# Performance work log

Hardware: AMD Instinct MI355X
Metric: run time of the kernel (lower is better)

Reference implementation:

```python
import jax, jax.numpy as jnp
import numpy as np

VOCAB, EMB, HID = 50000, 256, 512
BATCH, SEQ = 128, 512


def setup_inputs() -> dict:
    key = jax.random.key(0)
    k1, k2, k3, k4 = jax.random.split(key, 4)
    tokens = jax.random.randint(k1, (BATCH, SEQ), 0, VOCAB, dtype=jnp.int32)
    V = jax.random.normal(k2, (VOCAB, EMB), dtype=jnp.float32) * 0.05
    W = jax.random.normal(k3, (EMB + HID, HID), dtype=jnp.float32) * (1.0 / np.sqrt(EMB + HID))
    b = jnp.zeros((HID,), dtype=jnp.float32)
    Wd = jax.random.normal(k4, (HID, 1), dtype=jnp.float32) * (1.0 / np.sqrt(HID))
    bd = jnp.zeros((1,), dtype=jnp.float32)
    return {"tokens": tokens, "V": V, "W": W, "b": b, "Wd": Wd, "bd": bd}


def reference(tokens, V, W, b, Wd, bd):
    # embedding lookup: [B, S, E]
    x = V[tokens]
    B = x.shape[0]
    # tanh RNN over time: state_t = tanh([x_t, state_{t-1}] @ W + b)
    Wx, Wh = W[:EMB], W[EMB:]  # concat-matmul == split matmuls
    xs = jnp.einsum('bse,eh->bsh', x, Wx)  # precompute input projections

    def step(state, x_proj):
        state = jnp.tanh(x_proj + state @ Wh + b)
        return state, None

    init = jnp.zeros((B, HID), dtype=x.dtype)
    final_state, _ = jax.lax.scan(step, init, jnp.swapaxes(xs, 0, 1))
    # dense head -> [B]
    y = final_state @ Wd + bd
    return y.reshape(-1)
```

## Files before the change

kernel.cpp:

```cpp
#include <hip/hip_runtime.h>

#define EMBD 256
#define HIDD 512
#define SEQL 512
#define NCOL 512
#define CGC  64
#define THR  512
#define NRING 64
#define RPW  2

typedef unsigned int u32;
typedef unsigned long long u64;
typedef _Float16 h2 __attribute__((ext_vector_type(2)));

#define WS_W16_OFF 0
#define WS_X_OFF   (768 * 1024)

static __device__ __forceinline__ float dot2(u32 a, u32 b, float c) {
#if __has_builtin(__builtin_amdgcn_fdot2)
    return __builtin_amdgcn_fdot2(__builtin_bit_cast(h2, a), __builtin_bit_cast(h2, b), c, false);
#else
    h2 ha = __builtin_bit_cast(h2, a), hb = __builtin_bit_cast(h2, b);
    float r = fmaf((float)ha.x, (float)hb.x, c);
    return fmaf((float)ha.y, (float)hb.y, r);
#endif
}

static __device__ __forceinline__ u32 packh2(float a, float b) {
    _Float16 lo = (_Float16)a, hi = (_Float16)b;
    return (u32)__builtin_bit_cast(unsigned short, lo)
         | ((u32)__builtin_bit_cast(unsigned short, hi) << 16);
}

__global__ __launch_bounds__(1024)
void init_X(u64* __restrict__ X) {
    X[(size_t)blockIdx.x * 1024 + threadIdx.x] = 0ull;
}

__global__ __launch_bounds__(256)
void convert_W(const float* __restrict__ W, u32* __restrict__ W16) {
    int idx = blockIdx.x * 256 + threadIdx.x;
    if (idx >= 384 * NCOL) return;
    int kp = idx >> 9, c = idx & 511;
    float lo = W[(size_t)(2 * kp) * NCOL + c];
    float hi = W[(size_t)(2 * kp + 1) * NCOL + c];
    W16[idx] = packh2(lo, hi);
}

__global__ __launch_bounds__(THR, 1)
void rnn_ring(const int*   __restrict__ tokens,
              const float* __restrict__ V,
              const u32*   __restrict__ W16,
              const float* __restrict__ bias,
              const float* __restrict__ Wd,
              const float* __restrict__ bd,
              float*       __restrict__ y,
              u64*         __restrict__ X)
{
    __shared__ __align__(16) u32 vcA[RPW][384];
    __shared__ __align__(16) u32 vcB[RPW][384];
    __shared__ float partA[RPW][CGC][9];
    __shared__ float partB[RPW][CGC][9];
    __shared__ int   toks[4][SEQL];
    __shared__ float yred[8];

    const int tid  = threadIdx.x;
    const int wg   = blockIdx.x;
    const int pr   = wg >> 3;
    const int cg   = wg & 7;
    const int ringA = 2 * pr;
    const int wv   = tid >> 6;
    const int lane = tid & 63;
    const int gc   = cg * CGC + lane;
    const int row0 = pr * 4;

    for (int i = tid; i < 4 * SEQL; i += THR)
        toks[i >> 9][i & 511] = tokens[(row0 + (i >> 9)) * SEQL + (i & 511)];
    for (int i = tid; i < RPW * 256; i += THR) {
        vcA[i >> 8][128 + (i & 255)] = 0u;
        vcB[i >> 8][128 + (i & 255)] = 0u;
    }

    u32 we[16], ws[32];
    #pragma unroll
    for (int i = 0; i < 16; ++i) we[i] = W16[(size_t)(wv * 16 + i) * NCOL + gc];
    #pragma unroll
    for (int j = 0; j < 32; ++j) ws[j] = W16[(size_t)(128 + wv * 32 + j) * NCOL + gc];

    __syncthreads();

    const int er = tid >> 7, ee = tid & 127;
    {
        int tok = toks[er][0];
        float2 ev = *(const float2*)&V[(size_t)tok * EMBD + 2 * ee];
        u32 dw = packh2(ev.x, ev.y);
        if (er < 2) vcA[er][ee] = dw; else vcB[er - 2][ee] = dw;
    }
    __syncthreads();

    const float bias_r = (tid < 256) ? bias[cg * CGC + (tid & 63)] : 0.f;
    const int  lrow = lane >> 5, lpair = lane & 31;
    const bool own  = (wv == cg);
    const int  ringsel = tid >> 7, rrow = (tid >> 6) & 1, rcol = tid & 63;

    for (int t = 0; t < SEQL; ++t) {
        u64* XA = X + (((size_t)((t + 1) & 1) * NRING + ringA    ) * RPW + lrow) * 256 + wv * 32 + lpair;
        u64* XB = X + (((size_t)((t + 1) & 1) * NRING + ringA + 1) * RPW + lrow) * 256 + wv * 32 + lpair;
        u64 vA = 0, vB = 0;
        if (!own) {
            vA = __hip_atomic_load(XA, __ATOMIC_RELAXED, __HIP_MEMORY_SCOPE_AGENT);
            vB = __hip_atomic_load(XB, __ATOMIC_RELAXED, __HIP_MEMORY_SCOPE_AGENT);
        }

        const int tn   = (t + 1 < SEQL) ? (t + 1) : (SEQL - 1);
        const int tokn = toks[er][tn];
        const float2 ev = *(const float2*)&V[(size_t)tokn * EMBD + 2 * ee];

        float a0 = 0.f, a1 = 0.f, b0 = 0.f, b1 = 0.f;
        {
            const uint4* pa0 = (const uint4*)&vcA[0][wv * 16];
            const uint4* pa1 = (const uint4*)&vcA[1][wv * 16];
            const uint4* pb0 = (const uint4*)&vcB[0][wv * 16];
            const uint4* pb1 = (const uint4*)&vcB[1][wv * 16];
            #pragma unroll
            for (int j = 0; j < 4; ++j) {
                uint4 xa0 = pa0[j], xa1 = pa1[j], xb0 = pb0[j], xb1 = pb1[j];
                a0 = dot2(xa0.x, we[4*j+0], a0); a0 = dot2(xa0.y, we[4*j+1], a0);
                a0 = dot2(xa0.z, we[4*j+2], a0); a0 = dot2(xa0.w, we[4*j+3], a0);
                a1 = dot2(xa1.x, we[4*j+0], a1); a1 = dot2(xa1.y, we[4*j+1], a1);
                a1 = dot2(xa1.z, we[4*j+2], a1); a1 = dot2(xa1.w, we[4*j+3], a1);
                b0 = dot2(xb0.x, we[4*j+0], b0); b0 = dot2(xb0.y, we[4*j+1], b0);
                b0 = dot2(xb0.z, we[4*j+2], b0); b0 = dot2(xb0.w, we[4*j+3], b0);
                b1 = dot2(xb1.x, we[4*j+0], b1); b1 = dot2(xb1.y, we[4*j+1], b1);
                b1 = dot2(xb1.z, we[4*j+2], b1); b1 = dot2(xb1.w, we[4*j+3], b1);
            }
        }

        if (!own) {
            if (!__all((u32)(vA >> 32) == (u32)t)) {
                do {
                    __builtin_amdgcn_s_sleep(1);
                    vA = __hip_atomic_load(XA, __ATOMIC_RELAXED, __HIP_MEMORY_SCOPE_AGENT);
                } while (!__all((u32)(vA >> 32) == (u32)t));
            }
            vcA[lrow][128 + wv * 32 + lpair] = (u32)vA;
        }
        {
            const uint4* p0 = (const uint4*)&vcA[0][128 + wv * 32];
            const uint4* p1 = (const uint4*)&vcA[1][128 + wv * 32];
            #pragma unroll
            for (int j = 0; j < 8; ++j) {
                uint4 x0 = p0[j], x1 = p1[j];
                a0 = dot2(x0.x, ws[4*j+0], a0); a0 = dot2(x0.y, ws[4*j+1], a0);
                a0 = dot2(x0.z, ws[4*j+2], a0); a0 = dot2(x0.w, ws[4*j+3], a0);
                a1 = dot2(x1.x, ws[4*j+0], a1); a1 = dot2(x1.y, ws[4*j+1], a1);
                a1 = dot2(x1.z, ws[4*j+2], a1); a1 = dot2(x1.w, ws[4*j+3], a1);
            }
        }
        partA[0][lane][wv] = a0;
        partA[1][lane][wv] = a1;

        if (!own) {
            if (!__all((u32)(vB >> 32) == (u32)t)) {
                do {
                    __builtin_amdgcn_s_sleep(1);
                    vB = __hip_atomic_load(XB, __ATOMIC_RELAXED, __HIP_MEMORY_SCOPE_AGENT);
                } while (!__all((u32)(vB >> 32) == (u32)t));
            }
            vcB[lrow][128 + wv * 32 + lpair] = (u32)vB;
        }
        {
            const uint4* p0 = (const uint4*)&vcB[0][128 + wv * 32];
            const uint4* p1 = (const uint4*)&vcB[1][128 + wv * 32];
            #pragma unroll
            for (int j = 0; j < 8; ++j) {
                uint4 x0 = p0[j], x1 = p1[j];
                b0 = dot2(x0.x, ws[4*j+0], b0); b0 = dot2(x0.y, ws[4*j+1], b0);
                b0 = dot2(x0.z, ws[4*j+2], b0); b0 = dot2(x0.w, ws[4*j+3], b0);
                b1 = dot2(x1.x, ws[4*j+0], b1); b1 = dot2(x1.y, ws[4*j+1], b1);
                b1 = dot2(x1.z, ws[4*j+2], b1); b1 = dot2(x1.w, ws[4*j+3], b1);
            }
        }
        partB[0][lane][wv] = b0;
        partB[1][lane][wv] = b1;

        __syncthreads();

        if (tid < 256) {
            const float* P = ringsel ? &partB[rrow][rcol][0] : &partA[rrow][rcol][0];
            float s = P[0] + P[1] + P[2] + P[3] + P[4] + P[5] + P[6] + P[7] + bias_r;
            s = tanhf(s);
            float snb = __shfl_down(s, 1);
            if ((rcol & 1) == 0) {
                const int gp = cg * 32 + (rcol >> 1);
                u32 dw = packh2(s, snb);
                if (ringsel == 0) vcA[rrow][128 + gp] = dw;
                else              vcB[rrow][128 + gp] = dw;
                u64 pk = (u64)dw | ((u64)(u32)(t + 1) << 32);
                u64* dst = X + (((size_t)(t & 1) * NRING + ringA + ringsel) * RPW + rrow) * 256 + gp;
                __hip_atomic_store(dst, pk, __ATOMIC_RELAXED, __HIP_MEMORY_SCOPE_AGENT);
            }
        }
        {
            u32 dw = packh2(ev.x, ev.y);
            if (er < 2) vcA[er][ee] = dw; else vcB[er - 2][ee] = dw;
        }
        __syncthreads();
    }

    if (cg == 0) {
        if (wv != 0) {
            u64* XA = X + (((size_t)((SEQL - 1) & 1) * NRING + ringA    ) * RPW + lrow) * 256 + wv * 32 + lpair;
            u64* XB = X + (((size_t)((SEQL - 1) & 1) * NRING + ringA + 1) * RPW + lrow) * 256 + wv * 32 + lpair;
            u64 vA, vB;
            do {
                vA = __hip_atomic_load(XA, __ATOMIC_RELAXED, __HIP_MEMORY_SCOPE_AGENT);
            } while (!__all((u32)(vA >> 32) == (u32)SEQL));
            do {
                vB = __hip_atomic_load(XB, __ATOMIC_RELAXED, __HIP_MEMORY_SCOPE_AGENT);
            } while (!__all((u32)(vB >> 32) == (u32)SEQL));
            vcA[lrow][128 + wv * 32 + lpair] = (u32)vA;
            vcB[lrow][128 + wv * 32 + lpair] = (u32)vB;
        }
        __syncthreads();
        const int r = tid >> 7, q = tid & 127;
        u32 dA, dB;
        if (r < 2) { dA = vcA[r][128 + 2 * q];     dB = vcA[r][128 + 2 * q + 1]; }
        else       { dA = vcB[r - 2][128 + 2 * q]; dB = vcB[r - 2][128 + 2 * q + 1]; }
        h2 ha = __builtin_bit_cast(h2, dA), hb = __builtin_bit_cast(h2, dB);
        float p = (float)ha.x * Wd[4 * q + 0] + (float)ha.y * Wd[4 * q + 1]
                + (float)hb.x * Wd[4 * q + 2] + (float)hb.y * Wd[4 * q + 3];
        #pragma unroll
        for (int off = 32; off > 0; off >>= 1) p += __shfl_down(p, off);
        if ((tid & 63) == 0) yred[tid >> 6] = p;
        __syncthreads();
        if (tid < 4) y[row0 + tid] = yred[2 * tid] + yred[2 * tid + 1] + bd[0];
    }
}

extern "C" void kernel_launch(void* const* d_in, const int* in_sizes, int n_in,
                              void* d_out, int out_size, void* d_ws, size_t ws_size,
                              hipStream_t stream)
{
    const int*   tokens = (const int*)  d_in[0];
    const float* V      = (const float*)d_in[1];
    const float* W      = (const float*)d_in[2];
    const float* b      = (const float*)d_in[3];
    const float* Wd     = (const float*)d_in[4];
    const float* bd     = (const float*)d_in[5];
    float* y = (float*)d_out;

    u32* W16 = (u32*)((char*)d_ws + WS_W16_OFF);
    u64* X   = (u64*)((char*)d_ws + WS_X_OFF);

    hipLaunchKernelGGL(init_X, dim3(64), dim3(1024), 0, stream, X);
    hipLaunchKernelGGL(convert_W, dim3((384 * NCOL + 255) / 256), dim3(256), 0, stream, W, W16);
    hipLaunchKernelGGL(rnn_ring, dim3(256), dim3(THR), 0, stream,
                       tokens, V, W16, b, Wd, bd, y, X);
}
```

Before: 1.089 ms.

## Broadcast state and embedding via readlane instead of LDS vector staging

Keeps each wave's slice of the hidden state and embedding in a register (one packed half2 per lane) and broadcasts operands with readlane inside the dot-product loops, removing the shared-memory vcA/vcB staging buffers and their LDS reads. The own-block state is kept in a small LDS array, and the final dense head reads states directly from registers. This cuts LDS traffic and the store-then-load through shared memory on the recurrent critical path. In exchange it adds many scalar readlane operations per step, which may serialise on the scalar path.

```diff
diff --git a/kernel.cpp b/kernel.cpp
--- a/kernel.cpp
+++ b/kernel.cpp
@@ -1,10 +1,8 @@
 #include <hip/hip_runtime.h>
 
 #define EMBD 256
-#define HIDD 512
 #define SEQL 512
 #define NCOL 512
-#define CGC  64
 #define THR  512
 #define NRING 64
 #define RPW  2
@@ -32,6 +30,10 @@
          | ((u32)__builtin_bit_cast(unsigned short, hi) << 16);
 }
 
+static __device__ __forceinline__ u32 bcast(u32 v, int l) {
+    return (u32)__builtin_amdgcn_readlane((int)v, l);
+}
+
 __global__ __launch_bounds__(1024)
 void init_X(u64* __restrict__ X) {
     X[(size_t)blockIdx.x * 1024 + threadIdx.x] = 0ull;
@@ -48,38 +50,34 @@
 }
 
 __global__ __launch_bounds__(THR, 1)
-void rnn_ring(const int*   __restrict__ tokens,
-              const float* __restrict__ V,
-              const u32*   __restrict__ W16,
-              const float* __restrict__ bias,
-              const float* __restrict__ Wd,
-              const float* __restrict__ bd,
-              float*       __restrict__ y,
-              u64*         __restrict__ X)
+void rnn_rl(const int*   __restrict__ tokens,
+            const float* __restrict__ V,
+            const u32*   __restrict__ W16,
+            const float* __restrict__ bias,
+            const float* __restrict__ Wd,
+            const float* __restrict__ bd,
+            float*       __restrict__ y,
+            u64*         __restrict__ X)
 {
-    __shared__ __align__(16) u32 vcA[RPW][384];
-    __shared__ __align__(16) u32 vcB[RPW][384];
-    __shared__ float partA[RPW][CGC][9];
-    __shared__ float partB[RPW][CGC][9];
+    __shared__ float partA[RPW][64][9];
+    __shared__ float partB[RPW][64][9];
     __shared__ int   toks[4][SEQL];
-    __shared__ float yred[8];
-
-    const int tid  = threadIdx.x;
-    const int wg   = blockIdx.x;
-    const int pr   = wg >> 3;
-    const int cg   = wg & 7;
+    __shared__ u32   own[2][64];
+    __shared__ float yr[8][4];
+
+    const int tid   = threadIdx.x;
+    const int wg    = blockIdx.x;
+    const int pr    = wg >> 3;
+    const int cg    = wg & 7;
     const int ringA = 2 * pr;
-    const int wv   = tid >> 6;
-    const int lane = tid & 63;
-    const int gc   = cg * CGC + lane;
-    const int row0 = pr * 4;
+    const int wv    = tid >> 6;
+    const int lane  = tid & 63;
+    const int gc    = cg * 64 + lane;
+    const int row0  = pr * 4;
 
     for (int i = tid; i < 4 * SEQL; i += THR)
         toks[i >> 9][i & 511] = tokens[(row0 + (i >> 9)) * SEQL + (i & 511)];
-    for (int i = tid; i < RPW * 256; i += THR) {
-        vcA[i >> 8][128 + (i & 255)] = 0u;
-        vcB[i >> 8][128 + (i & 255)] = 0u;
-    }
+    if (tid < 128) own[tid >> 6][tid & 63] = 0u;
 
     u32 we[16], ws[32];
     #pragma unroll
@@ -89,101 +87,82 @@
 
     __syncthreads();
 
-    const int er = tid >> 7, ee = tid & 127;
+    const int erow  = lane >> 4;
+    const int gpair = wv * 16 + (lane & 15);
+    u32 em;
     {
-        int tok = toks[er][0];
-        float2 ev = *(const float2*)&V[(size_t)tok * EMBD + 2 * ee];
-        u32 dw = packh2(ev.x, ev.y);
-        if (er < 2) vcA[er][ee] = dw; else vcB[er - 2][ee] = dw;
+        int tok = toks[erow][0];
+        float2 e0 = *(const float2*)&V[(size_t)tok * EMBD + 2 * gpair];
+        em = packh2(e0.x, e0.y);
     }
-    __syncthreads();
-
-    const float bias_r = (tid < 256) ? bias[cg * CGC + (tid & 63)] : 0.f;
+
+    const float bias_r = (tid < 256) ? bias[cg * 64 + (tid & 63)] : 0.f;
     const int  lrow = lane >> 5, lpair = lane & 31;
-    const bool own  = (wv == cg);
+    const bool ownwv = (wv == cg);
     const int  ringsel = tid >> 7, rrow = (tid >> 6) & 1, rcol = tid & 63;
 
     for (int t = 0; t < SEQL; ++t) {
-        u64* XA = X + (((size_t)((t + 1) & 1) * NRING + ringA    ) * RPW + lrow) * 256 + wv * 32 + lpair;
-        u64* XB = X + (((size_t)((t + 1) & 1) * NRING + ringA + 1) * RPW + lrow) * 256 + wv * 32 + lpair;
+        const u64* XA = X + (((size_t)((t + 1) & 1) * NRING + ringA    ) * RPW + lrow) * 256 + wv * 32 + lpair;
+        const u64* XB = X + (((size_t)((t + 1) & 1) * NRING + ringA + 1) * RPW + lrow) * 256 + wv * 32 + lpair;
         u64 vA = 0, vB = 0;
-        if (!own) {
+        if (!ownwv) {
             vA = __hip_atomic_load(XA, __ATOMIC_RELAXED, __HIP_MEMORY_SCOPE_AGENT);
             vB = __hip_atomic_load(XB, __ATOMIC_RELAXED, __HIP_MEMORY_SCOPE_AGENT);
         }
 
         const int tn   = (t + 1 < SEQL) ? (t + 1) : (SEQL - 1);
-        const int tokn = toks[er][tn];
-        const float2 ev = *(const float2*)&V[(size_t)tokn * EMBD + 2 * ee];
+        const int tokn = toks[erow][tn];
+        const float2 ev = *(const float2*)&V[(size_t)tokn * EMBD + 2 * gpair];
 
         float a0 = 0.f, a1 = 0.f, b0 = 0.f, b1 = 0.f;
-        {
-            const uint4* pa0 = (const uint4*)&vcA[0][wv * 16];
-            const uint4* pa1 = (const uint4*)&vcA[1][wv * 16];
-            const uint4* pb0 = (const uint4*)&vcB[0][wv * 16];
-            const uint4* pb1 = (const uint4*)&vcB[1][wv * 16];
-            #pragma unroll
-            for (int j = 0; j < 4; ++j) {
-                uint4 xa0 = pa0[j], xa1 = pa1[j], xb0 = pb0[j], xb1 = pb1[j];
-                a0 = dot2(xa0.x, we[4*j+0], a0); a0 = dot2(xa0.y, we[4*j+1], a0);
-                a0 = dot2(xa0.z, we[4*j+2], a0); a0 = dot2(xa0.w, we[4*j+3], a0);
-                a1 = dot2(xa1.x, we[4*j+0], a1); a1 = dot2(xa1.y, we[4*j+1], a1);
-                a1 = dot2(xa1.z, we[4*j+2], a1); a1 = dot2(xa1.w, we[4*j+3], a1);
-                b0 = dot2(xb0.x, we[4*j+0], b0); b0 = dot2(xb0.y, we[4*j+1], b0);
-                b0 = dot2(xb0.z, we[4*j+2], b0); b0 = dot2(xb0.w, we[4*j+3], b0);
-                b1 = dot2(xb1.x, we[4*j+0], b1); b1 = dot2(xb1.y, we[4*j+1], b1);
-                b1 = dot2(xb1.z, we[4*j+2], b1); b1 = dot2(xb1.w, we[4*j+3], b1);
-            }
-        }
-
-        if (!own) {
+        #pragma unroll
+        for (int j = 0; j < 16; ++j) {
+            a0 = dot2(bcast(em,      j), we[j], a0);
+            a1 = dot2(bcast(em, 16 + j), we[j], a1);
+            b0 = dot2(bcast(em, 32 + j), we[j], b0);
+            b1 = dot2(bcast(em, 48 + j), we[j], b1);
+        }
+
+        u32 sA;
+        if (ownwv) {
+            sA = own[0][lane];
+        } else {
             if (!__all((u32)(vA >> 32) == (u32)t)) {
                 do {
                     __builtin_amdgcn_s_sleep(1);
                     vA = __hip_atomic_load(XA, __ATOMIC_RELAXED, __HIP_MEMORY_SCOPE_AGENT);
                 } while (!__all((u32)(vA >> 32) == (u32)t));
             }
-            vcA[lrow][128 + wv * 32 + lpair] = (u32)vA;
-        }
-        {
-            const uint4* p0 = (const uint4*)&vcA[0][128 + wv * 32];
-            const uint4* p1 = (const uint4*)&vcA[1][128 + wv * 32];
-            #pragma unroll
-            for (int j = 0; j < 8; ++j) {
-                uint4 x0 = p0[j], x1 = p1[j];
-                a0 = dot2(x0.x, ws[4*j+0], a0); a0 = dot2(x0.y, ws[4*j+1], a0);
-                a0 = dot2(x0.z, ws[4*j+2], a0); a0 = dot2(x0.w, ws[4*j+3], a0);
-                a1 = dot2(x1.x, ws[4*j+0], a1); a1 = dot2(x1.y, ws[4*j+1], a1);
-                a1 = dot2(x1.z, ws[4*j+2], a1); a1 = dot2(x1.w, ws[4*j+3], a1);
-            }
-        }
-        partA[0][lane][wv] = a0;
-        partA[1][lane][wv] = a1;
-
-        if (!own) {
+            sA = (u32)vA;
+        }
+        #pragma unroll
+        for (int p = 0; p < 32; ++p) {
+            a0 = dot2(bcast(sA,      p), ws[p], a0);
+            a1 = dot2(bcast(sA, 32 + p), ws[p], a1);
+        }
+
+        u32 sB;
+        if (ownwv) {
+            sB = own[1][lane];
+        } else {
             if (!__all((u32)(vB >> 32) == (u32)t)) {
                 do {
                     __builtin_amdgcn_s_sleep(1);
                     vB = __hip_atomic_load(XB, __ATOMIC_RELAXED, __HIP_MEMORY_SCOPE_AGENT);
                 } while (!__all((u32)(vB >> 32) == (u32)t));
             }
-            vcB[lrow][128 + wv * 32 + lpair] = (u32)vB;
-        }
-        {
-            const uint4* p0 = (const uint4*)&vcB[0][128 + wv * 32];
-            const uint4* p1 = (const uint4*)&vcB[1][128 + wv * 32];
-            #pragma unroll
-            for (int j = 0; j < 8; ++j) {
-                uint4 x0 = p0[j], x1 = p1[j];
-                b0 = dot2(x0.x, ws[4*j+0], b0); b0 = dot2(x0.y, ws[4*j+1], b0);
-                b0 = dot2(x0.z, ws[4*j+2], b0); b0 = dot2(x0.w, ws[4*j+3], b0);
-                b1 = dot2(x1.x, ws[4*j+0], b1); b1 = dot2(x1.y, ws[4*j+1], b1);
-                b1 = dot2(x1.z, ws[4*j+2], b1); b1 = dot2(x1.w, ws[4*j+3], b1);
-            }
-        }
+            sB = (u32)vB;
+        }
+        #pragma unroll
+        for (int p = 0; p < 32; ++p) {
+            b0 = dot2(bcast(sB,      p), ws[p], b0);
+            b1 = dot2(bcast(sB, 32 + p), ws[p], b1);
+        }
+
+        partA[0][lane][wv] = a0;
+        partA[1][lane][wv] = a1;
         partB[0][lane][wv] = b0;
         partB[1][lane][wv] = b1;
-
         __syncthreads();
 
         if (tid < 256) {
@@ -192,26 +171,26 @@
             s = tanhf(s);
             float snb = __shfl_down(s, 1);
             if ((rcol & 1) == 0) {
-                const int gp = cg * 32 + (rcol >> 1);
                 u32 dw = packh2(s, snb);
-                if (ringsel == 0) vcA[rrow][128 + gp] = dw;
-                else              vcB[rrow][128 + gp] = dw;
+                const int lp = rcol >> 1;
+                own[ringsel][rrow * 32 + lp] = dw;
                 u64 pk = (u64)dw | ((u64)(u32)(t + 1) << 32);
-                u64* dst = X + (((size_t)(t & 1) * NRING + ringA + ringsel) * RPW + rrow) * 256 + gp;
+                u64* dst = X + (((size_t)(t & 1) * NRING + ringA + ringsel) * RPW + rrow) * 256 + cg * 32 + lp;
                 __hip_atomic_store(dst, pk, __ATOMIC_RELAXED, __HIP_MEMORY_SCOPE_AGENT);
             }
         }
-        {
-            u32 dw = packh2(ev.x, ev.y);
-            if (er < 2) vcA[er][ee] = dw; else vcB[er - 2][ee] = dw;
-        }
+        em = packh2(ev.x, ev.y);
         __syncthreads();
     }
 
     if (cg == 0) {
-        if (wv != 0) {
-            u64* XA = X + (((size_t)((SEQL - 1) & 1) * NRING + ringA    ) * RPW + lrow) * 256 + wv * 32 + lpair;
-            u64* XB = X + (((size_t)((SEQL - 1) & 1) * NRING + ringA + 1) * RPW + lrow) * 256 + wv * 32 + lpair;
+        u32 dA, dB;
+        if (ownwv) {
+            dA = own[0][lane];
+            dB = own[1][lane];
+        } else {
+            const u64* XA = X + (((size_t)1 * NRING + ringA    ) * RPW + lrow) * 256 + wv * 32 + lpair;
+            const u64* XB = X + (((size_t)1 * NRING + ringA + 1) * RPW + lrow) * 256 + wv * 32 + lpair;
             u64 vA, vB;
             do {
                 vA = __hip_atomic_load(XA, __ATOMIC_RELAXED, __HIP_MEMORY_SCOPE_AGENT);
@@ -219,22 +198,29 @@
             do {
                 vB = __hip_atomic_load(XB, __ATOMIC_RELAXED, __HIP_MEMORY_SCOPE_AGENT);
             } while (!__all((u32)(vB >> 32) == (u32)SEQL));
-            vcA[lrow][128 + wv * 32 + lpair] = (u32)vA;
-            vcB[lrow][128 + wv * 32 + lpair] = (u32)vB;
-        }
+            dA = (u32)vA;
+            dB = (u32)vB;
+        }
+        const int h = 2 * (wv * 32 + lpair);
+        const float2 wd = *(const float2*)&Wd[h];
+        h2 ha = __builtin_bit_cast(h2, dA);
+        h2 hb = __builtin_bit_cast(h2, dB);
+        float pA = (float)ha.x * wd.x + (float)ha.y * wd.y;
+        float pB = (float)hb.x * wd.x + (float)hb.y * wd.y;
+        #pragma unroll
+        for (int off = 16; off > 0; off >>= 1) {
+            pA += __shfl_down(pA, off, 32);
+            pB += __shfl_down(pB, off, 32);
+        }
+        if (lane == 0)  { yr[wv][0] = pA; yr[wv][2] = pB; }
+        if (lane == 32) { yr[wv][1] = pA; yr[wv][3] = pB; }
         __syncthreads();
-        const int r = tid >> 7, q = tid & 127;
-        u32 dA, dB;
-        if (r < 2) { dA = vcA[r][128 + 2 * q];     dB = vcA[r][128 + 2 * q + 1]; }
-        else       { dA = vcB[r - 2][128 + 2 * q]; dB = vcB[r - 2][128 + 2 * q + 1]; }
-        h2 ha = __builtin_bit_cast(h2, dA), hb = __builtin_bit_cast(h2, dB);
-        float p = (float)ha.x * Wd[4 * q + 0] + (float)ha.y * Wd[4 * q + 1]
-                + (float)hb.x * Wd[4 * q + 2] + (float)hb.y * Wd[4 * q + 3];
-        #pragma unroll
-        for (int off = 32; off > 0; off >>= 1) p += __shfl_down(p, off);
-        if ((tid & 63) == 0) yred[tid >> 6] = p;
-        __syncthreads();
-        if (tid < 4) y[row0 + tid] = yred[2 * tid] + yred[2 * tid + 1] + bd[0];
+        if (tid < 4) {
+            float s = 0.f;
+            #pragma unroll
+            for (int w = 0; w < 8; ++w) s += yr[w][tid];
+            y[row0 + tid] = s + bd[0];
+        }
     }
 }
 
@@ -255,6 +241,6 @@
 
     hipLaunchKernelGGL(init_X, dim3(64), dim3(1024), 0, stream, X);
     hipLaunchKernelGGL(convert_W, dim3((384 * NCOL + 255) / 256), dim3(256), 0, stream, W, W16);
-    hipLaunchKernelGGL(rnn_ring, dim3(256), dim3(THR), 0, stream,
+    hipLaunchKernelGGL(rnn_rl, dim3(256), dim3(THR), 0, stream,
                        tokens, V, W16, b, Wd, bd, y, X);
 }
```

New measurement: 1.458 ms. 33.9% more time.
